# Optimization experiments

Measured on AMD Instinct MI355X. Metric: run time of the kernel, lower is better.

Reference implementation:

```python
import jax, jax.numpy as jnp
import numpy as np

B, S, H = 2, 2048, 2048
NH, HD = 16, 128
I = 8192
EPS = float(np.finfo(np.float32).eps)  # torch RMSNorm default eps=None -> dtype eps


def rmsnorm(x, w):
    var = jnp.mean(jnp.square(x), axis=-1, keepdims=True)
    return x * jax.lax.rsqrt(var + EPS) * w


def setup_inputs() -> dict:
    key = jax.random.key(0)
    ks = jax.random.split(key, 8)
    s = 0.02
    return {
        "hidden_states": jax.random.normal(ks[0], (B, S, H), jnp.float32),
        "Wq": jax.random.normal(ks[1], (H, H), jnp.float32) * s,
        "Wk": jax.random.normal(ks[2], (H, H), jnp.float32) * s,
        "Wv": jax.random.normal(ks[3], (H, H), jnp.float32) * s,
        "Wo": jax.random.normal(ks[4], (H, H), jnp.float32) * s,
        "Wg": jax.random.normal(ks[5], (I, H), jnp.float32) * s,
        "Wu": jax.random.normal(ks[6], (I, H), jnp.float32) * s,
        "Wd": jax.random.normal(ks[7], (H, I), jnp.float32) * s,
        "g_in": jnp.ones((H,), jnp.float32),
        "g_post": jnp.ones((H,), jnp.float32),
    }


def reference(hidden_states, Wq, Wk, Wv, Wo, Wg, Wu, Wd, g_in, g_post):
    residual = hidden_states
    x = rmsnorm(hidden_states, g_in)
    # projections: nn.Linear does x @ W.T
    q = (x @ Wq.T).reshape(B, S, NH, HD).transpose(0, 2, 1, 3)  # [B,NH,S,HD]
    k = (x @ Wk.T).reshape(B, S, NH, HD).transpose(0, 2, 1, 3)
    v = (x @ Wv.T).reshape(B, S, NH, HD).transpose(0, 2, 1, 3)
    scores = jnp.einsum("bhqd,bhkd->bhqk", q, k) / jnp.sqrt(jnp.float32(HD))
    attn = jax.nn.softmax(scores, axis=-1)
    out = jnp.einsum("bhqk,bhkd->bhqd", attn, v)
    out = out.transpose(0, 2, 1, 3).reshape(B, S, H)
    hidden_states = residual + out @ Wo.T
    residual = hidden_states
    x = rmsnorm(hidden_states, g_post)
    mlp = (jax.nn.silu(x @ Wg.T) * (x @ Wu.T)) @ Wd.T
    return residual + mlp
```

## Files before the change

kernel.cpp:

```cpp
#include <hip/hip_runtime.h>

using u16 = unsigned short;
using u32 = unsigned int;

typedef __attribute__((ext_vector_type(8))) __bf16 bf16x8;
typedef __attribute__((ext_vector_type(4))) float f32x4;

__device__ __forceinline__ u16 f2bf(float f) {
  __bf16 h = (__bf16)f;
  return __builtin_bit_cast(u16, h);
}
__device__ __forceinline__ u32 pk2(float a, float b) {
  return (u32)f2bf(a) | ((u32)f2bf(b) << 16);
}
__device__ __forceinline__ float bf2f(u16 h) {
  return __uint_as_float(((u32)h) << 16);
}
__device__ __forceinline__ void gload16(const u16* g, u16* l) {
  __builtin_amdgcn_global_load_lds((const __attribute__((address_space(1))) void*)g,
                                   (__attribute__((address_space(3))) void*)l, 16, 0, 0);
}
__device__ __forceinline__ f32x4 mfma_bf16(bf16x8 a, bf16x8 b, f32x4 c) {
  return __builtin_amdgcn_mfma_f32_16x16x32_bf16(a, b, c, 0, 0, 0);
}

__global__ __launch_bounds__(256) void cvt_bf16(const float* __restrict__ in,
                                                u16* __restrict__ out, int n8) {
  int i = blockIdx.x * 256 + threadIdx.x;
  int stride = gridDim.x * 256;
  for (; i < n8; i += stride) {
    float4 a = ((const float4*)in)[(size_t)i * 2];
    float4 b = ((const float4*)in)[(size_t)i * 2 + 1];
    ((uint4*)out)[i] = make_uint4(pk2(a.x, a.y), pk2(a.z, a.w), pk2(b.x, b.y), pk2(b.z, b.w));
  }
}

__global__ __launch_bounds__(256) void rmsnorm_bf16(const float* __restrict__ x,
                                                    const float* __restrict__ g,
                                                    u16* __restrict__ o) {
  const int row = blockIdx.x;
  const int tid = threadIdx.x;
  const float4* xr = (const float4*)(x + (size_t)row * 2048);
  float4 a = xr[tid * 2], b = xr[tid * 2 + 1];
  float s = a.x * a.x + a.y * a.y + a.z * a.z + a.w * a.w +
            b.x * b.x + b.y * b.y + b.z * b.z + b.w * b.w;
#pragma unroll
  for (int off = 1; off < 64; off <<= 1) s += __shfl_xor(s, off);
  __shared__ float red[4];
  if ((tid & 63) == 0) red[tid >> 6] = s;
  __syncthreads();
  s = red[0] + red[1] + red[2] + red[3];
  const float r = rsqrtf(s * (1.0f / 2048.0f) + 1.1920929e-07f);
  const float4* gr = (const float4*)g;
  float4 ga = gr[tid * 2], gb = gr[tid * 2 + 1];
  ((uint4*)(o + (size_t)row * 2048))[tid] =
      make_uint4(pk2(a.x * r * ga.x, a.y * r * ga.y), pk2(a.z * r * ga.z, a.w * r * ga.w),
                 pk2(b.x * r * gb.x, b.y * r * gb.y), pk2(b.z * r * gb.z, b.w * r * gb.w));
}

template <int EPI>
__global__ __launch_bounds__(512, 1) void gemm3b(const u16* __restrict__ A,
                                                 const u16* __restrict__ B,
                                                 u16* Cb, float* Cf,
                                                 const float* __restrict__ Res,
                                                 int M, int N, int K, int lda) {
  constexpr int BUF = 24576;
  alignas(16) __shared__ u16 lds[3 * BUF];
  const int tid = threadIdx.x;
  const int w = tid >> 6, lane = tid & 63;
  const int lo = lane & 15, hi = lane >> 4;

  const int nbm = M >> 8, nbx = N >> 7;
  const int RM = nbm >> 1, RN = nbx >> 2;
  const int xcd = blockIdx.x & 7, idx = blockIdx.x >> 3;
  const int bm = ((xcd >> 2) * RM + idx / RN) << 8;
  const int bn = ((xcd & 3) * RN + idx % RN) << 7;

  const int wm = w >> 1, wn = w & 1;

  const int scol = ((tid & 7) ^ ((tid >> 3) & 7)) * 8;
  const u16* Ag = A + (size_t)(bm + (tid >> 3)) * lda + scol;
  const u16* Bg = B + (size_t)(bn + (tid >> 3)) * K + scol;

  f32x4 acc[4][4] = {};

#define STG(b, kt)                                                                    \
  {                                                                                   \
    _Pragma("unroll") for (int c = 0; c < 4; ++c)                                     \
        gload16(Ag + (size_t)(c * 64) * lda + (kt), &lds[(b)*BUF + c * 4096 + tid * 8]); \
    _Pragma("unroll") for (int c = 0; c < 2; ++c)                                     \
        gload16(Bg + (size_t)(c * 64) * K + (kt), &lds[(b)*BUF + 16384 + c * 4096 + tid * 8]); \
  }

  const int NT = K >> 6;
  STG(0, 0);
  STG(1, 64);

  int cur = 0;
  for (int T = 0; T < NT; ++T) {
    if (T + 1 < NT) {
      asm volatile("s_waitcnt vmcnt(6)" ::: "memory");
    } else {
      asm volatile("s_waitcnt vmcnt(0)" ::: "memory");
    }
    __builtin_amdgcn_s_barrier();
    __builtin_amdgcn_sched_barrier(0);

    const u16* LA = &lds[cur * BUF];
    const u16* LB = LA + 16384;
    bf16x8 af[4][2], bf[4][2];
#pragma unroll
    for (int ks = 0; ks < 2; ++ks) {
#pragma unroll
      for (int m = 0; m < 4; ++m)
        af[m][ks] = *(const bf16x8*)(LA + (wm * 64 + m * 16 + lo) * 64 +
                                     ((ks * 4 + hi) ^ (lo & 7)) * 8);
#pragma unroll
      for (int n = 0; n < 4; ++n)
        bf[n][ks] = *(const bf16x8*)(LB + (wn * 64 + n * 16 + lo) * 64 +
                                     ((ks * 4 + hi) ^ (lo & 7)) * 8);
    }
    if (T + 2 < NT) {
      const int nb = (cur + 2) % 3;
      STG(nb, (T + 2) << 6);
    }
    __builtin_amdgcn_s_setprio(1);
#pragma unroll
    for (int ks = 0; ks < 2; ++ks)
#pragma unroll
      for (int m = 0; m < 4; ++m)
#pragma unroll
        for (int n = 0; n < 4; ++n) acc[m][n] = mfma_bf16(af[m][ks], bf[n][ks], acc[m][n]);
    __builtin_amdgcn_s_setprio(0);
    cur = (cur + 1) % 3;
  }
#undef STG

#pragma unroll
  for (int m = 0; m < 4; ++m) {
    const int gr = bm + wm * 64 + m * 16 + hi * 4;
#pragma unroll
    for (int n = 0; n < 4; ++n) {
      const int gc = bn + wn * 64 + n * 16 + lo;
#pragma unroll
      for (int r = 0; r < 4; ++r) {
        const size_t idx2 = (size_t)(gr + r) * N + gc;
        if constexpr (EPI == 1) {
          Cf[idx2] = Res[idx2] + acc[m][n][r];
        } else if constexpr (EPI == 2) {
          float g = bf2f(Cb[idx2]);
          float s = g / (1.f + __expf(-g));
          Cb[idx2] = f2bf(s * acc[m][n][r]);
        } else {
          Cb[idx2] = f2bf(acc[m][n][r]);
        }
      }
    }
  }
}

template <int EPI>
__global__ __launch_bounds__(256) void gemm_bt(const u16* __restrict__ A,
                                               const float* __restrict__ B,
                                               u16* Cb, float* Cf, const float* Res,
                                               int M, int N, int K) {
  alignas(16) __shared__ u16 As[128 * 32];
  alignas(16) __shared__ u16 Bs[128 * 32];
  const int tid = threadIdx.x;
  const int w = tid >> 6, lane = tid & 63;
  const int lo = lane & 15, hi = lane >> 4;
  const int bm = blockIdx.y * 128, bn = blockIdx.x * 128;
  const int wr = (w >> 1) * 64, wc = (w & 1) * 64;
  f32x4 acc[4][4] = {};
  const int r0 = tid >> 2, kc0 = (tid & 3) * 8;
  const u16* a0 = A + (size_t)(bm + r0) * K + kc0;
  const u16* a1 = A + (size_t)(bm + 64 + r0) * K + kc0;
  const float* b0 = B + (size_t)(bn + r0) * K + kc0;
  const float* b1 = B + (size_t)(bn + 64 + r0) * K + kc0;
  u16* asd0 = &As[(size_t)tid * 8];
  u16* asd1 = &As[(size_t)(tid + 256) * 8];
  u16* bsd0 = &Bs[(size_t)tid * 8];
  u16* bsd1 = &Bs[(size_t)(tid + 256) * 8];
  for (int kt = 0; kt < K; kt += 32) {
    gload16(a0 + kt, asd0);
    gload16(a1 + kt, asd1);
    float4 x0 = *(const float4*)(b0 + kt);
    float4 x1 = *(const float4*)(b0 + kt + 4);
    float4 y0 = *(const float4*)(b1 + kt);
    float4 y1 = *(const float4*)(b1 + kt + 4);
    *(uint4*)bsd0 = make_uint4(pk2(x0.x, x0.y), pk2(x0.z, x0.w), pk2(x1.x, x1.y), pk2(x1.z, x1.w));
    *(uint4*)bsd1 = make_uint4(pk2(y0.x, y0.y), pk2(y0.z, y0.w), pk2(y1.x, y1.y), pk2(y1.z, y1.w));
    __syncthreads();
    bf16x8 af[4], bfr[4];
#pragma unroll
    for (int i = 0; i < 4; ++i) {
      af[i] = *(const bf16x8*)(&As[(wr + i * 16 + lo) * 32 + hi * 8]);
      bfr[i] = *(const bf16x8*)(&Bs[(wc + i * 16 + lo) * 32 + hi * 8]);
    }
#pragma unroll
    for (int i = 0; i < 4; ++i)
#pragma unroll
      for (int j = 0; j < 4; ++j) acc[i][j] = mfma_bf16(af[i], bfr[j], acc[i][j]);
    __syncthreads();
  }
#pragma unroll
  for (int i = 0; i < 4; ++i) {
    const int gr = bm + wr + i * 16 + hi * 4;
#pragma unroll
    for (int j = 0; j < 4; ++j) {
      const int gc = bn + wc + j * 16 + lo;
#pragma unroll
      for (int r = 0; r < 4; ++r) {
        const size_t idx = (size_t)(gr + r) * N + gc;
        if constexpr (EPI == 1) {
          Cf[idx] = Res[idx] + acc[i][j][r];
        } else if constexpr (EPI == 2) {
          float g = bf2f(Cb[idx]);
          float s = g / (1.f + __expf(-g));
          Cb[idx] = f2bf(s * acc[i][j][r]);
        } else {
          Cb[idx] = f2bf(acc[i][j][r]);
        }
      }
    }
  }
}

__global__ __launch_bounds__(256) void transpose_v(const u16* __restrict__ v,
                                                   u16* __restrict__ vt, int ldv) {
  __shared__ u16 t[32][33];
  const int bh = blockIdx.z, b = bh >> 4, h = bh & 15;
  const int s0 = blockIdx.x * 32, d0 = blockIdx.y * 32;
  const int tx = threadIdx.x, ty = threadIdx.y;
#pragma unroll
  for (int i = 0; i < 4; ++i)
    t[ty + i * 8][tx] = v[(size_t)(b * 2048 + s0 + ty + i * 8) * ldv + h * 128 + d0 + tx];
  __syncthreads();
#pragma unroll
  for (int i = 0; i < 4; ++i)
    vt[(size_t)(bh * 128 + d0 + ty + i * 8) * 2048 + s0 + tx] = t[tx][ty + i * 8];
}

__global__ __launch_bounds__(256) void attn_fwd2(const u16* __restrict__ q,
                                                 const u16* __restrict__ k,
                                                 const u16* __restrict__ vt,
                                                 u16* o, int ldq) {
  constexpr int S = 2048;
  alignas(16) __shared__ u16 Ks[2][64 * 128];
  alignas(16) __shared__ u16 Vs[2][128 * 64];
  alignas(16) __shared__ u16 plds[4][16 * 72];
  const int bh = blockIdx.y, b = bh >> 4, h = bh & 15;
  const int tid = threadIdx.x, w = tid >> 6, lane = tid & 63;
  const int lo = lane & 15, hi = lane >> 4;
  const int qr = blockIdx.x * 64 + w * 16;
  u16* pl = &plds[w][0];

  bf16x8 qf[4];
  const u16* qb = q + (size_t)(b * S + qr + lo) * ldq + h * 128 + hi * 8;
#pragma unroll
  for (int ks = 0; ks < 4; ++ks) qf[ks] = *(const bf16x8*)(qb + ks * 32);

  f32x4 oacc[8] = {};
  float m[4], l[4];
#pragma unroll
  for (int r = 0; r < 4; ++r) { m[r] = -1e30f; l[r] = 0.f; }

  const u16* kb = k + (size_t)(b * S) * ldq + h * 128;
  const u16* vb = vt + (size_t)bh * 128 * S;

  const int kcs = ((((tid & 15) * 16) ^ (((tid >> 4) & 7) << 4)) >> 1);
  const int vcs = ((((tid & 7) * 16) ^ (((tid >> 3) & 7) << 4)) >> 1);
  const u16* kgs = kb + (size_t)(tid >> 4) * ldq + kcs;
  const u16* vgs = vb + (size_t)(tid >> 3) * S + vcs;

  int cur = 0;
#pragma unroll
  for (int c = 0; c < 4; ++c) gload16(kgs + (size_t)(c * 16) * ldq, &Ks[0][c * 2048 + tid * 8]);
#pragma unroll
  for (int c = 0; c < 4; ++c) gload16(vgs + (size_t)(c * 32) * S, &Vs[0][c * 2048 + tid * 8]);
  __syncthreads();

  const int swq = (lo & 7) << 4;
  constexpr float SCL = 0.12752956f;

  for (int kv = 0; kv < S; kv += 64) {
    if (kv + 64 < S) {
      const int nb = cur ^ 1;
#pragma unroll
      for (int c = 0; c < 4; ++c)
        gload16(kgs + (size_t)(kv + 64 + c * 16) * ldq, &Ks[nb][c * 2048 + tid * 8]);
#pragma unroll
      for (int c = 0; c < 4; ++c)
        gload16(vgs + (size_t)(c * 32) * S + kv + 64, &Vs[nb][c * 2048 + tid * 8]);
    }
    const u16* Kc = &Ks[cur][0];
    const u16* Vc = &Vs[cur][0];

    f32x4 sacc[4] = {};
    __builtin_amdgcn_s_setprio(1);
#pragma unroll
    for (int ks = 0; ks < 4; ++ks)
#pragma unroll
      for (int n = 0; n < 4; ++n) {
        bf16x8 kf = *(const bf16x8*)(Kc + (n * 16 + lo) * 128 + (((ks * 64 + hi * 16) ^ swq) >> 1));
        sacc[n] = mfma_bf16(qf[ks], kf, sacc[n]);
      }
    __builtin_amdgcn_s_setprio(0);

    float mv[4];
#pragma unroll
    for (int r = 0; r < 4; ++r)
      mv[r] = fmaxf(fmaxf(sacc[0][r], sacc[1][r]), fmaxf(sacc[2][r], sacc[3][r]));
#pragma unroll
    for (int off = 1; off < 16; off <<= 1)
#pragma unroll
      for (int r = 0; r < 4; ++r) mv[r] = fmaxf(mv[r], __shfl_xor(mv[r], off));

    bool need = false;
#pragma unroll
    for (int r = 0; r < 4; ++r) need = need || (mv[r] > m[r] + 62.f);
    if (__any(need)) {
#pragma unroll
      for (int r = 0; r < 4; ++r) {
        float nm = fmaxf(m[r], mv[r]);
        float c = exp2f((m[r] - nm) * SCL);
        m[r] = nm;
        l[r] *= c;
#pragma unroll
        for (int f = 0; f < 8; ++f) oacc[f][r] *= c;
      }
    }
    float mm[4];
#pragma unroll
    for (int r = 0; r < 4; ++r) mm[r] = m[r] * SCL;

    f32x4 p[4];
#pragma unroll
    for (int n = 0; n < 4; ++n)
#pragma unroll
      for (int r = 0; r < 4; ++r) p[n][r] = exp2f(fmaf(sacc[n][r], SCL, -mm[r]));
    float ps[4];
#pragma unroll
    for (int r = 0; r < 4; ++r) ps[r] = (p[0][r] + p[1][r]) + (p[2][r] + p[3][r]);
#pragma unroll
    for (int off = 1; off < 16; off <<= 1)
#pragma unroll
      for (int r = 0; r < 4; ++r) ps[r] += __shfl_xor(ps[r], off);
#pragma unroll
    for (int r = 0; r < 4; ++r) l[r] += ps[r];

#pragma unroll
    for (int n = 0; n < 4; ++n)
#pragma unroll
      for (int r = 0; r < 4; ++r)
        pl[(hi * 4 + r) * 72 + n * 16 + lo] = f2bf(p[n][r]);
    asm volatile("s_waitcnt lgkmcnt(0)" ::: "memory");
    bf16x8 pf0 = *(const bf16x8*)(pl + lo * 72 + hi * 8);
    bf16x8 pf1 = *(const bf16x8*)(pl + lo * 72 + 32 + hi * 8);

    __builtin_amdgcn_s_setprio(1);
#pragma unroll
    for (int f = 0; f < 8; ++f) {
      const int row = f * 16 + lo;
      bf16x8 vf0 = *(const bf16x8*)(Vc + row * 64 + (((hi * 16) ^ swq) >> 1));
      bf16x8 vf1 = *(const bf16x8*)(Vc + row * 64 + (((64 + hi * 16) ^ swq) >> 1));
      oacc[f] = mfma_bf16(pf0, vf0, oacc[f]);
      oacc[f] = mfma_bf16(pf1, vf1, oacc[f]);
    }
    __builtin_amdgcn_s_setprio(0);

    __syncthreads();
    cur ^= 1;
  }

  u16* ob = o + (size_t)(b * S + qr) * ldq + h * 128;
#pragma unroll
  for (int f = 0; f < 8; ++f)
#pragma unroll
    for (int r = 0; r < 4; ++r)
      ob[(size_t)(hi * 4 + r) * ldq + f * 16 + lo] = f2bf(oacc[f][r] / l[r]);
}

extern "C" void kernel_launch(void* const* d_in, const int* in_sizes, int n_in,
                              void* d_out, int out_size, void* d_ws, size_t ws_size,
                              hipStream_t stream) {
  constexpr int B = 2, S = 2048, H = 2048, NH = 16, I = 8192;
  constexpr int M = B * S;

  const float* hs = (const float*)d_in[0];
  const float* Wq = (const float*)d_in[1];
  const float* Wk = (const float*)d_in[2];
  const float* Wv = (const float*)d_in[3];
  const float* Wo = (const float*)d_in[4];
  const float* Wg = (const float*)d_in[5];
  const float* Wu = (const float*)d_in[6];
  const float* Wd = (const float*)d_in[7];
  const float* g_in = (const float*)d_in[8];
  const float* g_post = (const float*)d_in[9];
  float* out = (float*)d_out;

  constexpr size_t SZ_HH = (size_t)H * H * 2;
  constexpr size_t SZ_IH = (size_t)I * H * 2;
  constexpr size_t SZ_MH = (size_t)M * H * 2;
  constexpr size_t NEED_NEW = SZ_MH + 3 * SZ_MH + SZ_MH + SZ_IH;

  if (ws_size >= NEED_NEW) {
    char* p = (char*)d_ws;
    u16* x_b = (u16*)p;    p += SZ_MH;
    u16* qkv_b = (u16*)p;  p += 3 * SZ_MH;
    u16* vt_b = (u16*)p;   p += SZ_MH;
    u16* wsc = (u16*)p;    p += SZ_IH;
    u16* gate_b = qkv_b;

    rmsnorm_bf16<<<M, 256, 0, stream>>>(hs, g_in, x_b);

    cvt_bf16<<<1024, 256, 0, stream>>>(Wq, wsc, H * H / 8);
    cvt_bf16<<<1024, 256, 0, stream>>>(Wk, wsc + (size_t)H * H, H * H / 8);
    cvt_bf16<<<1024, 256, 0, stream>>>(Wv, wsc + (size_t)2 * H * H, H * H / 8);
    gemm3b<0><<<(M / 256) * (3 * H / 128), 512, 0, stream>>>(
        x_b, wsc, qkv_b, nullptr, nullptr, M, 3 * H, H, H);

    transpose_v<<<dim3(S / 32, 128 / 32, B * NH), dim3(32, 8), 0, stream>>>(
        qkv_b + 2 * H, vt_b, 3 * H);
    attn_fwd2<<<dim3(S / 64, B * NH), 256, 0, stream>>>(qkv_b, qkv_b + H, vt_b, qkv_b, 3 * H);

    cvt_bf16<<<1024, 256, 0, stream>>>(Wo, wsc, H * H / 8);
    gemm3b<1><<<(M / 256) * (H / 128), 512, 0, stream>>>(
        qkv_b, wsc, nullptr, out, hs, M, H, H, 3 * H);

    rmsnorm_bf16<<<M, 256, 0, stream>>>(out, g_post, x_b);

    cvt_bf16<<<1024, 256, 0, stream>>>(Wg, wsc, I * H / 8);
    gemm3b<0><<<(M / 256) * (I / 128), 512, 0, stream>>>(
        x_b, wsc, gate_b, nullptr, nullptr, M, I, H, H);
    cvt_bf16<<<1024, 256, 0, stream>>>(Wu, wsc, I * H / 8);
    gemm3b<2><<<(M / 256) * (I / 128), 512, 0, stream>>>(
        x_b, wsc, gate_b, nullptr, nullptr, M, I, H, H);
    cvt_bf16<<<1024, 256, 0, stream>>>(Wd, wsc, I * H / 8);
    gemm3b<1><<<(M / 256) * (H / 128), 512, 0, stream>>>(
        gate_b, wsc, nullptr, out, out, M, H, I, I);
    return;
  }

  constexpr int MC = 2048;
  char* p = (char*)d_ws;
  u16* x_b = (u16*)p;   p += SZ_MH;
  u16* q_b = (u16*)p;   p += SZ_MH;
  u16* k_b = (u16*)p;   p += SZ_MH;
  u16* v_b = (u16*)p;   p += SZ_MH;
  u16* vt_b = (u16*)p;  p += SZ_MH;
  u16* g_mlp = k_b;

  rmsnorm_bf16<<<M, 256, 0, stream>>>(hs, g_in, x_b);
  const dim3 gHH(H / 128, M / 128);
  gemm_bt<0><<<gHH, 256, 0, stream>>>(x_b, Wq, q_b, nullptr, nullptr, M, H, H);
  gemm_bt<0><<<gHH, 256, 0, stream>>>(x_b, Wk, k_b, nullptr, nullptr, M, H, H);
  gemm_bt<0><<<gHH, 256, 0, stream>>>(x_b, Wv, v_b, nullptr, nullptr, M, H, H);
  transpose_v<<<dim3(S / 32, 128 / 32, B * NH), dim3(32, 8), 0, stream>>>(v_b, vt_b, H);
  attn_fwd2<<<dim3(S / 64, B * NH), 256, 0, stream>>>(q_b, k_b, vt_b, q_b, H);
  gemm_bt<1><<<gHH, 256, 0, stream>>>(q_b, Wo, nullptr, out, hs, M, H, H);
  rmsnorm_bf16<<<M, 256, 0, stream>>>(out, g_post, x_b);
  const dim3 gIH(I / 128, MC / 128), gHI(H / 128, MC / 128);
  for (int mc = 0; mc < M / MC; ++mc) {
    const u16* xc = x_b + (size_t)mc * MC * H;
    float* oc = out + (size_t)mc * MC * H;
    gemm_bt<0><<<gIH, 256, 0, stream>>>(xc, Wg, g_mlp, nullptr, nullptr, MC, I, H);
    gemm_bt<2><<<gIH, 256, 0, stream>>>(xc, Wu, g_mlp, nullptr, nullptr, MC, I, H);
    gemm_bt<1><<<gHI, 256, 0, stream>>>(g_mlp, Wd, nullptr, oc, oc, MC, H, I);
  }
}
```

Before: 855.0 us.

## Add 256x256-tile GEMM with k-half pipelining; defer attention row-sum reduction

```diff
diff --git a/kernel.cpp b/kernel.cpp
--- a/kernel.cpp
+++ b/kernel.cpp
@@ -59,6 +59,128 @@
 }
 
 template <int EPI>
+__global__ __launch_bounds__(512, 2) void gemm4p(const u16* __restrict__ A,
+                                                 const u16* __restrict__ B,
+                                                 u16* Cb, float* Cf,
+                                                 const float* __restrict__ Res,
+                                                 int M, int N, int K, int lda) {
+  alignas(16) __shared__ u16 lds[8 * 8192];
+  const int tid = threadIdx.x;
+  const int w = tid >> 6, lane = tid & 63;
+  const int lo = lane & 15, hi = lane >> 4;
+  const int nbm = M >> 8, nbx = N >> 8;
+  const int RM = nbm >> 1, RN = nbx >> 2;
+  const int xcd = blockIdx.x & 7, bidx = blockIdx.x >> 3;
+  const int bm = ((xcd >> 2) * RM + bidx / RN) << 8;
+  const int bn = ((xcd & 3) * RN + bidx % RN) << 8;
+  const int wm = w >> 2, wn = w & 3;
+
+  const int rw = (hi ^ ((lo >> 1) & 3)) * 8;
+  const int arow0 = wm * 128 + lo, brow0 = wn * 64 + lo;
+
+  const int srow = tid >> 2;
+  const int scol = ((tid & 3) ^ ((tid >> 3) & 3)) * 8;
+  const u16* Ab = A + (size_t)(bm + srow) * lda + scol;
+  const u16* Bb = B + (size_t)(bn + srow) * K + scol;
+
+  f32x4 acc[8][4] = {};
+  bf16x8 af[4], bf[4];
+
+#define SLOT(par, kh, op) ((((par) * 2 + (kh)) * 2 + (op)) * 8192)
+#define STG(par, kh, op, kt)                                                   \
+  {                                                                            \
+    const u16* g_ = (op) ? Bb : Ab;                                            \
+    const int ld_ = (op) ? K : lda;                                            \
+    gload16(g_ + (kt) + (kh) * 32, &lds[SLOT(par, kh, op) + tid * 8]);         \
+    gload16(g_ + (size_t)128 * ld_ + (kt) + (kh) * 32,                         \
+            &lds[SLOT(par, kh, op) + 4096 + tid * 8]);                         \
+  }
+#define MFMA16(mb)                                                             \
+  __builtin_amdgcn_s_setprio(1);                                               \
+  _Pragma("unroll") for (int m_ = 0; m_ < 4; ++m_)                             \
+      _Pragma("unroll") for (int n_ = 0; n_ < 4; ++n_)                         \
+          acc[m_ + (mb)][n_] = mfma_bf16(af[m_], bf[n_], acc[m_ + (mb)][n_]);  \
+  __builtin_amdgcn_s_setprio(0);
+#define BAR()                       \
+  __builtin_amdgcn_s_barrier();     \
+  __builtin_amdgcn_sched_barrier(0);
+
+  STG(0, 0, 0, 0); STG(0, 0, 1, 0); STG(0, 1, 0, 0); STG(0, 1, 1, 0);
+  asm volatile("s_waitcnt vmcnt(0)" ::: "memory");
+  BAR();
+
+  const int NT = K >> 6;
+  for (int t = 0; t < NT; ++t) {
+    const int par = t & 1, np = par ^ 1;
+    const int ktn = (t + 1) << 6;
+    const bool pre = (t + 1 < NT);
+    const u16* LA0 = &lds[SLOT(par, 0, 0)];
+    const u16* LB0 = &lds[SLOT(par, 0, 1)];
+    const u16* LA1 = &lds[SLOT(par, 1, 0)];
+    const u16* LB1 = &lds[SLOT(par, 1, 1)];
+
+#pragma unroll
+    for (int n = 0; n < 4; ++n) bf[n] = *(const bf16x8*)(LB0 + (brow0 + n * 16) * 32 + rw);
+#pragma unroll
+    for (int m = 0; m < 4; ++m) af[m] = *(const bf16x8*)(LA0 + (arow0 + m * 16) * 32 + rw);
+    if (pre) STG(np, 0, 0, ktn);
+    MFMA16(0);
+    BAR();
+
+#pragma unroll
+    for (int m = 0; m < 4; ++m)
+      af[m] = *(const bf16x8*)(LA0 + (arow0 + (m + 4) * 16) * 32 + rw);
+    if (pre) STG(np, 0, 1, ktn);
+    MFMA16(4);
+    if (pre) { asm volatile("s_waitcnt vmcnt(4)" ::: "memory"); }
+    else     { asm volatile("s_waitcnt vmcnt(0)" ::: "memory"); }
+    BAR();
+
+#pragma unroll
+    for (int n = 0; n < 4; ++n) bf[n] = *(const bf16x8*)(LB1 + (brow0 + n * 16) * 32 + rw);
+#pragma unroll
+    for (int m = 0; m < 4; ++m) af[m] = *(const bf16x8*)(LA1 + (arow0 + m * 16) * 32 + rw);
+    if (pre) STG(np, 1, 0, ktn);
+    MFMA16(0);
+    BAR();
+
+#pragma unroll
+    for (int m = 0; m < 4; ++m)
+      af[m] = *(const bf16x8*)(LA1 + (arow0 + (m + 4) * 16) * 32 + rw);
+    if (pre) STG(np, 1, 1, ktn);
+    MFMA16(4);
+    if (pre) { asm volatile("s_waitcnt vmcnt(4)" ::: "memory"); }
+    BAR();
+  }
+#undef SLOT
+#undef STG
+#undef MFMA16
+#undef BAR
+
+#pragma unroll
+  for (int m = 0; m < 8; ++m) {
+    const int gr = bm + wm * 128 + m * 16 + hi * 4;
+#pragma unroll
+    for (int n = 0; n < 4; ++n) {
+      const int gc = bn + wn * 64 + n * 16 + lo;
+#pragma unroll
+      for (int r = 0; r < 4; ++r) {
+        const size_t idx = (size_t)(gr + r) * N + gc;
+        if constexpr (EPI == 1) {
+          Cf[idx] = Res[idx] + acc[m][n][r];
+        } else if constexpr (EPI == 2) {
+          float g = bf2f(Cb[idx]);
+          float s = g / (1.f + __expf(-g));
+          Cb[idx] = f2bf(s * acc[m][n][r]);
+        } else {
+          Cb[idx] = f2bf(acc[m][n][r]);
+        }
+      }
+    }
+  }
+}
+
+template <int EPI>
 __global__ __launch_bounds__(512, 1) void gemm3b(const u16* __restrict__ A,
                                                  const u16* __restrict__ B,
                                                  u16* Cb, float* Cf,
@@ -77,7 +199,6 @@
   const int bn = ((xcd & 3) * RN + idx % RN) << 7;
 
   const int wm = w >> 1, wn = w & 1;
-
   const int scol = ((tid & 7) ^ ((tid >> 3) & 7)) * 8;
   const u16* Ag = A + (size_t)(bm + (tid >> 3)) * lda + scol;
   const u16* Bg = B + (size_t)(bn + (tid >> 3)) * K + scol;
@@ -248,7 +369,7 @@
   constexpr int S = 2048;
   alignas(16) __shared__ u16 Ks[2][64 * 128];
   alignas(16) __shared__ u16 Vs[2][128 * 64];
-  alignas(16) __shared__ u16 plds[4][16 * 72];
+  alignas(16) __shared__ u16 plds[4][16 * 68];
   const int bh = blockIdx.y, b = bh >> 4, h = bh & 15;
   const int tid = threadIdx.x, w = tid >> 6, lane = tid & 63;
   const int lo = lane & 15, hi = lane >> 4;
@@ -261,9 +382,10 @@
   for (int ks = 0; ks < 4; ++ks) qf[ks] = *(const bf16x8*)(qb + ks * 32);
 
   f32x4 oacc[8] = {};
-  float m[4], l[4];
-#pragma unroll
-  for (int r = 0; r < 4; ++r) { m[r] = -1e30f; l[r] = 0.f; }
+  float m[4];
+  f32x4 lp = {0.f, 0.f, 0.f, 0.f};
+#pragma unroll
+  for (int r = 0; r < 4; ++r) m[r] = -1e30f;
 
   const u16* kb = k + (size_t)(b * S) * ldq + h * 128;
   const u16* vb = vt + (size_t)bh * 128 * S;
@@ -325,7 +447,7 @@
         float nm = fmaxf(m[r], mv[r]);
         float c = exp2f((m[r] - nm) * SCL);
         m[r] = nm;
-        l[r] *= c;
+        lp[r] *= c;
 #pragma unroll
         for (int f = 0; f < 8; ++f) oacc[f][r] *= c;
       }
@@ -339,24 +461,18 @@
     for (int n = 0; n < 4; ++n)
 #pragma unroll
       for (int r = 0; r < 4; ++r) p[n][r] = exp2f(fmaf(sacc[n][r], SCL, -mm[r]));
-    float ps[4];
-#pragma unroll
-    for (int r = 0; r < 4; ++r) ps[r] = (p[0][r] + p[1][r]) + (p[2][r] + p[3][r]);
-#pragma unroll
-    for (int off = 1; off < 16; off <<= 1)
-#pragma unroll
-      for (int r = 0; r < 4; ++r) ps[r] += __shfl_xor(ps[r], off);
-#pragma unroll
-    for (int r = 0; r < 4; ++r) l[r] += ps[r];
+#pragma unroll
+    for (int r = 0; r < 4; ++r)
+      lp[r] += (p[0][r] + p[1][r]) + (p[2][r] + p[3][r]);
 
 #pragma unroll
     for (int n = 0; n < 4; ++n)
 #pragma unroll
       for (int r = 0; r < 4; ++r)
-        pl[(hi * 4 + r) * 72 + n * 16 + lo] = f2bf(p[n][r]);
+        pl[(hi * 4 + r) * 68 + n * 16 + lo] = f2bf(p[n][r]);
     asm volatile("s_waitcnt lgkmcnt(0)" ::: "memory");
-    bf16x8 pf0 = *(const bf16x8*)(pl + lo * 72 + hi * 8);
-    bf16x8 pf1 = *(const bf16x8*)(pl + lo * 72 + 32 + hi * 8);
+    bf16x8 pf0 = *(const bf16x8*)(pl + lo * 68 + hi * 8);
+    bf16x8 pf1 = *(const bf16x8*)(pl + lo * 68 + 32 + hi * 8);
 
     __builtin_amdgcn_s_setprio(1);
 #pragma unroll
@@ -372,6 +488,14 @@
     __syncthreads();
     cur ^= 1;
   }
+
+  float l[4];
+#pragma unroll
+  for (int r = 0; r < 4; ++r) l[r] = lp[r];
+#pragma unroll
+  for (int off = 1; off < 16; off <<= 1)
+#pragma unroll
+    for (int r = 0; r < 4; ++r) l[r] += __shfl_xor(l[r], off);
 
   u16* ob = o + (size_t)(b * S + qr) * ldq + h * 128;
 #pragma unroll
@@ -417,7 +541,7 @@
     cvt_bf16<<<1024, 256, 0, stream>>>(Wq, wsc, H * H / 8);
     cvt_bf16<<<1024, 256, 0, stream>>>(Wk, wsc + (size_t)H * H, H * H / 8);
     cvt_bf16<<<1024, 256, 0, stream>>>(Wv, wsc + (size_t)2 * H * H, H * H / 8);
-    gemm3b<0><<<(M / 256) * (3 * H / 128), 512, 0, stream>>>(
+    gemm4p<0><<<(M / 256) * (3 * H / 256), 512, 0, stream>>>(
         x_b, wsc, qkv_b, nullptr, nullptr, M, 3 * H, H, H);
 
     transpose_v<<<dim3(S / 32, 128 / 32, B * NH), dim3(32, 8), 0, stream>>>(
@@ -431,10 +555,10 @@
     rmsnorm_bf16<<<M, 256, 0, stream>>>(out, g_post, x_b);
 
     cvt_bf16<<<1024, 256, 0, stream>>>(Wg, wsc, I * H / 8);
-    gemm3b<0><<<(M / 256) * (I / 128), 512, 0, stream>>>(
+    gemm4p<0><<<(M / 256) * (I / 256), 512, 0, stream>>>(
         x_b, wsc, gate_b, nullptr, nullptr, M, I, H, H);
     cvt_bf16<<<1024, 256, 0, stream>>>(Wu, wsc, I * H / 8);
-    gemm3b<2><<<(M / 256) * (I / 128), 512, 0, stream>>>(
+    gemm4p<2><<<(M / 256) * (I / 256), 512, 0, stream>>>(
         x_b, wsc, gate_b, nullptr, nullptr, M, I, H, H);
     cvt_bf16<<<1024, 256, 0, stream>>>(Wd, wsc, I * H / 8);
     gemm3b<1><<<(M / 256) * (H / 128), 512, 0, stream>>>(
```

New measurement: 873.2 us. 2.1% more time.
